# Kernel optimization log

Hardware: AMD Instinct MI355X
Metric: run time of the kernel (lower is better)

The kernel has to match this reference:

```python
import jax, jax.numpy as jnp
import numpy as np


def _conv2d(x, w, stride, padding):
    # x: NCHW, w: OIHW
    return jax.lax.conv_general_dilated(
        x, w, window_strides=(stride, stride),
        padding=((padding, padding), (padding, padding)),
        dimension_numbers=('NCHW', 'OIHW', 'NCHW'))


def setup_inputs() -> dict:
    key = jax.random.key(0)
    k1, k2 = jax.random.split(key)
    B, C_in, H, Wd = 8, 64, 256, 256
    C_out, ksz = 64, 3
    x = jax.random.normal(k1, (B, C_in, H, Wd), dtype=jnp.float32)
    W = jax.random.normal(k2, (C_out, C_in, ksz, ksz), dtype=jnp.float32)
    b = jnp.zeros((C_out,), dtype=jnp.float32)
    return {"x": x, "W": W, "b": b}


def reference(x, W, b):
    stride, padding = 1, 1
    B, C, H, Wd = x.shape
    # per-pixel (across-channel) normalization of activations
    xf = jnp.transpose(x, (0, 2, 3, 1)).reshape(-1, C)       # [B*H*W, C]
    mu = jnp.mean(xf, axis=-1, keepdims=True)
    var = jnp.mean((xf - mu) ** 2, axis=-1, keepdims=True)    # unbiased=False
    r = 1.0 / jnp.sqrt(var + 1e-8)
    y_norm = r * (xf - mu)
    # int8 fake-quant per pixel
    s_act = 127.0 / jnp.maximum(jnp.max(jnp.abs(y_norm), axis=-1, keepdims=True), 1e-8)
    y_tilde = jnp.clip(jnp.round(s_act * y_norm), -128.0, 127.0) / s_act
    y4 = jnp.transpose(y_tilde.reshape(B, H, Wd, C), (0, 3, 1, 2))
    # ternary weight quant (value; STE only matters for backward)
    s_w = 1.0 / jnp.maximum(jnp.mean(jnp.abs(W)), 1e-8)
    w_tilde = jnp.clip(jnp.round(s_w * W), -1.0, 1.0) / s_w
    out = _conv2d(y4, w_tilde, stride, padding) + b[None, :, None, None]
    return out
```

## Files before the change

kernel.cpp:

```cpp
#include <hip/hip_runtime.h>

typedef _Float16 half8 __attribute__((ext_vector_type(8)));
typedef float    f32x4 __attribute__((ext_vector_type(4)));

#define NB   8
#define NC   64
#define NH   256
#define NW   256
#define NO   64
#define TW_OFF   0ull
#define TW_BYTES (576ull * 64ull * 2ull)
#define MSW_OFF  (TW_OFF + TW_BYTES)

__global__ __launch_bounds__(256) void wq_kernel(const float* __restrict__ W,
                                                 _Float16* __restrict__ tw2,
                                                 float* __restrict__ msw_out) {
    __shared__ float red[256];
    __shared__ float sw_sh;
    int tid = threadIdx.x;
    float s = 0.0f;
    #pragma unroll
    for (int i = 0; i < 144; ++i) s += fabsf(W[i * 256 + tid]);
    red[tid] = s;
    __syncthreads();
    for (int off = 128; off > 0; off >>= 1) {
        if (tid < off) red[tid] += red[tid + off];
        __syncthreads();
    }
    if (tid == 0) {
        float mean = red[0] / 36864.0f;
        float msw  = fmaxf(mean, 1e-8f);
        sw_sh      = 1.0f / msw;
        msw_out[0] = msw;
    }
    __syncthreads();
    float s_w = sw_sh;
    #pragma unroll
    for (int i = 0; i < 144; ++i) {
        int idx = i * 256 + tid;
        float t = rintf(s_w * W[idx]);
        t = fminf(1.0f, fmaxf(-1.0f, t));
        int o  = idx / 576;
        int r  = idx - o * 576;
        int c  = r / 9;
        int r2 = r - c * 9;
        int kh = r2 / 3;
        int kw = r2 - kh * 3;
        int k  = (kh * 3 + kw) * 64 + c;
        tw2[((k >> 3) * 64 + o) * 8 + (k & 7)] = (_Float16)t;
    }
}

__global__ __launch_bounds__(256, 3) void fused_kernel(const float* __restrict__ x,
                                                       const _Float16* __restrict__ tw2,
                                                       const float* __restrict__ msw_p,
                                                       const float* __restrict__ bias,
                                                       float* __restrict__ out) {
    __shared__ alignas(16) _Float16 lds[3 * 8 * 66 * 8];

    int tid = threadIdx.x;
    int pb  = blockIdx.x;
    int bid = (pb & 7) * 1024 + (pb >> 3);
    int wt = bid & 3;
    int h  = (bid >> 2) & 255;
    int bb = bid >> 10;
    int w0 = wt * 64;

    if (tid < 198) {
        int kh = tid / 66;
        int wl = tid - kh * 66;
        int hp = h + kh - 1;
        int wp = w0 + wl - 1;
        float v[64];
        float s = 0.0f;
        if ((unsigned)hp < 256u && (unsigned)wp < 256u) {
            const float* xp = x + (size_t)bb * 64 * 65536 + (size_t)hp * 256 + wp;
            #pragma unroll
            for (int c = 0; c < 64; ++c) { v[c] = xp[(size_t)c * 65536]; s += v[c]; }
        } else {
            #pragma unroll
            for (int c = 0; c < 64; ++c) v[c] = 0.0f;
        }
        float mu = s * (1.0f / 64.0f);
        float var = 0.0f, dmax = 0.0f;
        #pragma unroll
        for (int c = 0; c < 64; ++c) {
            float d = v[c] - mu;
            var += d * d;
            dmax = fmaxf(dmax, fabsf(d));
        }
        var *= (1.0f / 64.0f);
        float r    = 1.0f / sqrtf(var + 1e-8f);
        float amax = fmaxf(dmax * r, 1e-8f);
        float s_a  = 127.0f / amax;
        float invs = amax / 127.0f;
        #pragma unroll
        for (int cc = 0; cc < 8; ++cc) {
            half8 hv;
            #pragma unroll
            for (int j = 0; j < 8; ++j) {
                float yn = (v[cc * 8 + j] - mu) * r;
                float q  = rintf(s_a * yn);
                q = fminf(127.0f, fmaxf(-128.0f, q));
                hv[j] = (_Float16)(q * invs);
            }
            *(half8*)(lds + ((kh * 8 + cc) * 66 + wl) * 8) = hv;
        }
    }

    int l   = tid & 63;
    int wv  = tid >> 6;
    int l15 = l & 15;
    int q8  = l >> 4;

    half8 aw[18];
    #pragma unroll
    for (int ks = 0; ks < 18; ++ks)
        aw[ks] = *(const half8*)(tw2 + (((ks * 4 + q8) * 64) + wv * 16 + l15) * 8);

    __syncthreads();

    f32x4 acc[4];
    #pragma unroll
    for (int nt = 0; nt < 4; ++nt)
        #pragma unroll
        for (int r2 = 0; r2 < 4; ++r2) acc[nt][r2] = 0.0f;

    #pragma unroll
    for (int ks = 0; ks < 18; ++ks) {
        int tap = ks >> 1;
        int kh  = tap / 3;
        int kw  = tap - kh * 3;
        int ccb = (ks & 1) * 4 + q8;
        int base = ((kh * 8 + ccb) * 66 + kw + l15) * 8;
        #pragma unroll
        for (int nt = 0; nt < 4; ++nt) {
            half8 bf = *(const half8*)(lds + base + nt * 128);
            acc[nt] = __builtin_amdgcn_mfma_f32_16x16x32_f16(aw[ks], bf, acc[nt], 0, 0, 0);
        }
    }

    float msw = *msw_p;
    size_t obase = ((size_t)bb * 64) * 65536 + (size_t)h * 256;
    #pragma unroll
    for (int reg = 0; reg < 4; ++reg) {
        int o = wv * 16 + q8 * 4 + reg;
        float bo = bias[o];
        #pragma unroll
        for (int nt = 0; nt < 4; ++nt) {
            int w = w0 + nt * 16 + l15;
            out[obase + (size_t)o * 65536 + w] = acc[nt][reg] * msw + bo;
        }
    }
}

extern "C" void kernel_launch(void* const* d_in, const int* in_sizes, int n_in,
                              void* d_out, int out_size, void* d_ws, size_t ws_size,
                              hipStream_t stream) {
    const float* x = (const float*)d_in[0];
    const float* W = (const float*)d_in[1];
    const float* b = (const float*)d_in[2];
    float* out = (float*)d_out;

    char* ws = (char*)d_ws;
    _Float16* tw2 = (_Float16*)(ws + TW_OFF);
    float*    msw = (float*)(ws + MSW_OFF);

    wq_kernel<<<1, 256, 0, stream>>>(W, tw2, msw);
    fused_kernel<<<8192, 256, 0, stream>>>(x, tw2, msw, b, out);
}
```

Measured before the change: 330.0 us.

## Stage raw activations in LDS with single-pass stats; parallelize weight quantization

The fused kernel no longer holds all 64 channel values in a register array. It computes sum, sum of squares, min and max in one pass, writes the raw values as fp16 to LDS, then re-reads them from LDS to normalize and quantize. This lowers register pressure so the launch bound can ask for 4 waves per SIMD instead of 3. The single-block weight quantization is split into a 144-block partial-sum kernel and a 144-block quantize kernel, which adds one launch. Risks: rounding the raw values to fp16 before normalizing and using the E[x^2]-mu^2 variance can change the int8 quantization boundaries.

```diff
diff --git a/kernel.cpp b/kernel.cpp
--- a/kernel.cpp
+++ b/kernel.cpp
@@ -11,47 +11,52 @@
 #define TW_OFF   0ull
 #define TW_BYTES (576ull * 64ull * 2ull)
 #define MSW_OFF  (TW_OFF + TW_BYTES)
+#define PART_OFF (MSW_OFF + 16ull)
 
-__global__ __launch_bounds__(256) void wq_kernel(const float* __restrict__ W,
-                                                 _Float16* __restrict__ tw2,
-                                                 float* __restrict__ msw_out) {
+__global__ __launch_bounds__(256) void wsum_kernel(const float* __restrict__ W,
+                                                   float* __restrict__ partial) {
     __shared__ float red[256];
-    __shared__ float sw_sh;
     int tid = threadIdx.x;
-    float s = 0.0f;
-    #pragma unroll
-    for (int i = 0; i < 144; ++i) s += fabsf(W[i * 256 + tid]);
-    red[tid] = s;
+    red[tid] = fabsf(W[blockIdx.x * 256 + tid]);
     __syncthreads();
     for (int off = 128; off > 0; off >>= 1) {
         if (tid < off) red[tid] += red[tid + off];
         __syncthreads();
     }
-    if (tid == 0) {
-        float mean = red[0] / 36864.0f;
-        float msw  = fmaxf(mean, 1e-8f);
-        sw_sh      = 1.0f / msw;
-        msw_out[0] = msw;
-    }
-    __syncthreads();
-    float s_w = sw_sh;
-    #pragma unroll
-    for (int i = 0; i < 144; ++i) {
-        int idx = i * 256 + tid;
-        float t = rintf(s_w * W[idx]);
-        t = fminf(1.0f, fmaxf(-1.0f, t));
-        int o  = idx / 576;
-        int r  = idx - o * 576;
-        int c  = r / 9;
-        int r2 = r - c * 9;
-        int kh = r2 / 3;
-        int kw = r2 - kh * 3;
-        int k  = (kh * 3 + kw) * 64 + c;
-        tw2[((k >> 3) * 64 + o) * 8 + (k & 7)] = (_Float16)t;
-    }
+    if (tid == 0) partial[blockIdx.x] = red[0];
 }
 
-__global__ __launch_bounds__(256, 3) void fused_kernel(const float* __restrict__ x,
+__global__ __launch_bounds__(256) void wq2_kernel(const float* __restrict__ W,
+                                                  const float* __restrict__ partial,
+                                                  _Float16* __restrict__ tw2,
+                                                  float* __restrict__ msw_out) {
+    __shared__ float red[256];
+    int tid = threadIdx.x;
+    red[tid] = (tid < 144) ? partial[tid] : 0.0f;
+    __syncthreads();
+    for (int off = 128; off > 0; off >>= 1) {
+        if (tid < off) red[tid] += red[tid + off];
+        __syncthreads();
+    }
+    float mean = red[0] / 36864.0f;
+    float msw  = fmaxf(mean, 1e-8f);
+    float s_w  = 1.0f / msw;
+    if (blockIdx.x == 0 && tid == 0) msw_out[0] = msw;
+
+    int idx = blockIdx.x * 256 + tid;
+    float t = rintf(s_w * W[idx]);
+    t = fminf(1.0f, fmaxf(-1.0f, t));
+    int o  = idx / 576;
+    int r  = idx - o * 576;
+    int c  = r / 9;
+    int r2 = r - c * 9;
+    int kh = r2 / 3;
+    int kw = r2 - kh * 3;
+    int k  = (kh * 3 + kw) * 64 + c;
+    tw2[((k >> 3) * 64 + o) * 8 + (k & 7)] = (_Float16)t;
+}
+
+__global__ __launch_bounds__(256, 4) void fused_kernel(const float* __restrict__ x,
                                                        const _Float16* __restrict__ tw2,
                                                        const float* __restrict__ msw_p,
                                                        const float* __restrict__ bias,
@@ -71,35 +76,41 @@
         int wl = tid - kh * 66;
         int hp = h + kh - 1;
         int wp = w0 + wl - 1;
-        float v[64];
-        float s = 0.0f;
-        if ((unsigned)hp < 256u && (unsigned)wp < 256u) {
-            const float* xp = x + (size_t)bb * 64 * 65536 + (size_t)hp * 256 + wp;
-            #pragma unroll
-            for (int c = 0; c < 64; ++c) { v[c] = xp[(size_t)c * 65536]; s += v[c]; }
-        } else {
-            #pragma unroll
-            for (int c = 0; c < 64; ++c) v[c] = 0.0f;
-        }
-        float mu = s * (1.0f / 64.0f);
-        float var = 0.0f, dmax = 0.0f;
-        #pragma unroll
-        for (int c = 0; c < 64; ++c) {
-            float d = v[c] - mu;
-            var += d * d;
-            dmax = fmaxf(dmax, fabsf(d));
-        }
-        var *= (1.0f / 64.0f);
-        float r    = 1.0f / sqrtf(var + 1e-8f);
-        float amax = fmaxf(dmax * r, 1e-8f);
-        float s_a  = 127.0f / amax;
-        float invs = amax / 127.0f;
+        int inb = ((unsigned)hp < 256u) & ((unsigned)wp < 256u);
+        int hpc = min(max(hp, 0), 255);
+        int wpc = min(max(wp, 0), 255);
+        const float* xp = x + (size_t)bb * 64 * 65536 + (size_t)hpc * 256 + wpc;
+        float fin = (float)inb;
+
+        float s = 0.0f, sq = 0.0f, mn = 1e30f, mx = -1e30f;
         #pragma unroll
         for (int cc = 0; cc < 8; ++cc) {
             half8 hv;
             #pragma unroll
             for (int j = 0; j < 8; ++j) {
-                float yn = (v[cc * 8 + j] - mu) * r;
+                float v = xp[(size_t)(cc * 8 + j) * 65536] * fin;
+                s  += v;
+                sq += v * v;
+                mn = fminf(mn, v);
+                mx = fmaxf(mx, v);
+                hv[j] = (_Float16)v;
+            }
+            *(half8*)(lds + ((kh * 8 + cc) * 66 + wl) * 8) = hv;
+        }
+        float mu  = s * (1.0f / 64.0f);
+        float var = fmaxf(sq * (1.0f / 64.0f) - mu * mu, 0.0f);
+        float r    = 1.0f / sqrtf(var + 1e-8f);
+        float dmax = fmaxf(mx - mu, mu - mn);
+        float amax = fmaxf(dmax * r, 1e-8f);
+        float s_a  = 127.0f / amax;
+        float invs = amax / 127.0f;
+
+        #pragma unroll
+        for (int cc = 0; cc < 8; ++cc) {
+            half8 hv = *(half8*)(lds + ((kh * 8 + cc) * 66 + wl) * 8);
+            #pragma unroll
+            for (int j = 0; j < 8; ++j) {
+                float yn = ((float)hv[j] - mu) * r;
                 float q  = rintf(s_a * yn);
                 q = fminf(127.0f, fmaxf(-128.0f, q));
                 hv[j] = (_Float16)(q * invs);
@@ -163,9 +174,11 @@
     float* out = (float*)d_out;
 
     char* ws = (char*)d_ws;
-    _Float16* tw2 = (_Float16*)(ws + TW_OFF);
-    float*    msw = (float*)(ws + MSW_OFF);
+    _Float16* tw2  = (_Float16*)(ws + TW_OFF);
+    float*    msw  = (float*)(ws + MSW_OFF);
+    float*    part = (float*)(ws + PART_OFF);
 
-    wq_kernel<<<1, 256, 0, stream>>>(W, tw2, msw);
+    wsum_kernel<<<144, 256, 0, stream>>>(W, part);
+    wq2_kernel<<<144, 256, 0, stream>>>(W, part, tw2, msw);
     fused_kernel<<<8192, 256, 0, stream>>>(x, tw2, msw, b, out);
 }
```

New measurement: 313.5 us. 5.0% less time.
